# Performance work log

Hardware: AMD Instinct MI355X
Metric: run time of the kernel (lower is better)

## Reference

```python
import jax, jax.numpy as jnp
import numpy as np

NUM_BANDS = 8
WINDOW = 2048
OVERLAP = 1024
SR = 16000


def _band_mask(L):
    # Replicates torch: band = searchsorted(band_ranges, |freq|, left) - 1.
    # DC bin gives band=-1 which torch negative-indexes into the LAST band,
    # hence the mod. All bins satisfy band < NUM_BANDS, so all are assigned.
    freqs = np.fft.fftfreq(L, 1.0 / SR)
    ranges = np.linspace(0.0, SR / 2.0, NUM_BANDS + 1)
    idx = np.searchsorted(ranges, np.abs(freqs), side='left') - 1
    idx = idx % NUM_BANDS
    mask = (idx[None, :] == np.arange(NUM_BANDS)[:, None]).astype(np.float32)
    return jnp.asarray(mask)  # [bands, L]


def _band_signals(x):
    # mag*exp(i*phase) of masked bins == masked complex bins; ifft().real per band
    L = x.shape[-1]
    X = jnp.fft.fft(x)                         # [B, L] complex
    mask = _band_mask(L)                       # [bands, L]
    Xb = X[:, None, :] * mask[None, :, :]      # [B, bands, L]
    return jnp.fft.ifft(Xb).real               # [B, bands, L]


def _chunks(sig):
    L = sig.shape[-1]
    hop = WINDOW - OVERLAP
    n = (L - OVERLAP) // hop                   # num_chunks (static)
    idx = (jnp.arange(n) * hop)[:, None] + jnp.arange(WINDOW)[None, :]  # [n, W]
    return sig[:, :, idx]                       # [B, bands, n, W]


def _loudness(x):
    # BS.1770-style energy loudness (vectorized stand-in for the repo's
    # undefined `loudness` helper): -0.691 + 10*log10(mean square)
    ms = jnp.mean(x * x, axis=-1)
    return -0.691 + 10.0 * jnp.log10(ms + 1e-12)


def reference(watermarked_signals, original_signals):
    ro = _band_signals(original_signals)
    rw = _band_signals(watermarked_signals)
    lo = _loudness(_chunks(ro))                # [B, bands, n]
    lw = _loudness(_chunks(rw))
    lo = jnp.where(jnp.isnan(lo), 0.0, lo)
    lw = jnp.where(jnp.isnan(lw), 0.0, lw)
    diff = (lw - lo).reshape(-1)               # ordered (i, j, k) like the torch loop
    w = jax.nn.softmax(diff)
    return jnp.sum(w * diff)


def setup_inputs() -> dict:
    key = jax.random.key(0)
    k1, k2 = jax.random.split(key)
    B, L = 8, 160000
    return {
        'watermarked_signals': jax.random.normal(k1, (B, L), dtype=jnp.float32),
        'original_signals': jax.random.normal(k2, (B, L), dtype=jnp.float32),
    }
```

## Files before the change

kernel.cpp:

```cpp
#include <hip/hip_runtime.h>
#include <hip/hip_fp16.h>
#include <math.h>

constexpr int L      = 160000;
constexpr int BATCH  = 8;
constexpr int NB     = 8;
constexpr int NHOPS  = 156;
constexpr int NCHUNK = 155;
constexpr int RS     = 289;
constexpr float TWO_PI = 6.28318530717958647692f;
constexpr float INVL = 1.0f / (float)L;

__device__ __forceinline__ float2 cmulf(float2 a, float2 b) {
  return make_float2(a.x * b.x - a.y * b.y, a.x * b.y + a.y * b.x);
}

__device__ __forceinline__ float2 cisf(float a) {
  float s, c;
  __sincosf(a, &s, &c);
  return make_float2(c, s);
}

__device__ __forceinline__ float2 conjf(float2 a) { return make_float2(a.x, -a.y); }

__device__ __forceinline__ int pad8(int i) { return i + (i >> 3); }

template <int SIGN>
__device__ __forceinline__ void bf4s(float2* v) {
  float2 t0 = make_float2(v[0].x + v[2].x, v[0].y + v[2].y);
  float2 t1 = make_float2(v[0].x - v[2].x, v[0].y - v[2].y);
  float2 t2 = make_float2(v[1].x + v[3].x, v[1].y + v[3].y);
  float2 t3 = make_float2(v[1].x - v[3].x, v[1].y - v[3].y);
  v[0] = make_float2(t0.x + t2.x, t0.y + t2.y);
  v[2] = make_float2(t0.x - t2.x, t0.y - t2.y);
  if constexpr (SIGN < 0) {
    v[1] = make_float2(t1.x + t3.y, t1.y - t3.x);
    v[3] = make_float2(t1.x - t3.y, t1.y + t3.x);
  } else {
    v[1] = make_float2(t1.x - t3.y, t1.y + t3.x);
    v[3] = make_float2(t1.x + t3.y, t1.y - t3.x);
  }
}

template <int SIGN>
__device__ __forceinline__ void bf5s(float2* v) {
  const float c1 = 0.30901699437494745f, s1 = 0.9510565162951535f;
  const float c2 = -0.8090169943749475f, s2 = 0.5877852522924731f;
  float2 t1 = make_float2(v[1].x + v[4].x, v[1].y + v[4].y);
  float2 t3 = make_float2(v[1].x - v[4].x, v[1].y - v[4].y);
  float2 t2 = make_float2(v[2].x + v[3].x, v[2].y + v[3].y);
  float2 t4 = make_float2(v[2].x - v[3].x, v[2].y - v[3].y);
  float2 a = make_float2(v[0].x + c1 * t1.x + c2 * t2.x, v[0].y + c1 * t1.y + c2 * t2.y);
  float2 b = make_float2(s1 * t3.x + s2 * t4.x, s1 * t3.y + s2 * t4.y);
  float2 c = make_float2(v[0].x + c2 * t1.x + c1 * t2.x, v[0].y + c2 * t1.y + c1 * t2.y);
  float2 d = make_float2(s2 * t3.x - s1 * t4.x, s2 * t3.y - s1 * t4.y);
  v[0] = make_float2(v[0].x + t1.x + t2.x, v[0].y + t1.y + t2.y);
  if constexpr (SIGN < 0) {
    v[1] = make_float2(a.x + b.y, a.y - b.x);
    v[4] = make_float2(a.x - b.y, a.y + b.x);
    v[2] = make_float2(c.x + d.y, c.y - d.x);
    v[3] = make_float2(c.x - d.y, c.y + d.x);
  } else {
    v[1] = make_float2(a.x - b.y, a.y + b.x);
    v[4] = make_float2(a.x + b.y, a.y - b.x);
    v[2] = make_float2(c.x - d.y, c.y + d.x);
    v[3] = make_float2(c.x + d.y, c.y - d.x);
  }
}

template <int R>
__device__ __forceinline__ void twchain(float2* v, float2 t1) {
  float2 t = t1;
  v[1] = cmulf(v[1], t);
#pragma unroll
  for (int r = 2; r < R; ++r) { t = cmulf(t, t1); v[r] = cmulf(v[r], t); }
}

__device__ __forceinline__ int rev3_5(int q) {
  int q5 = q / 5, q25 = q / 25;
  int d0 = q - 5 * q5, d1 = q5 - 5 * q25;
  return 25 * d0 + 5 * d1 + q25;
}

__device__ __forceinline__ int rev3_4(int q) {
  return ((q & 3) << 4) | (q & 12) | (q >> 4);
}

template <int SUB, int SIGN>
__device__ __forceinline__ void dif5_stage_1b(float2* a, int idx) {
  int j = idx % SUB;
  int b = (idx / SUB) * (5 * SUB) + j;
  float2 u[5];
#pragma unroll
  for (int r = 0; r < 5; ++r) u[r] = a[b + SUB * r];
  bf5s<SIGN>(u);
  twchain<5>(u, cisf((float)SIGN * (TWO_PI / (float)(5 * SUB)) * (float)j));
#pragma unroll
  for (int r = 0; r < 5; ++r) a[b + SUB * r] = u[r];
}

template <int SUB>
__device__ __forceinline__ void dif5_ip_stage_t(float2* a, int ln, float2 t1a, float2 t1b) {
  int i1 = ln, i2 = ln + 64;
  bool g2 = (i2 < 125);
  int j1 = i1 % SUB, j2 = i2 % SUB;
  int b1 = (i1 / SUB) * (5 * SUB) + j1;
  int b2 = (i2 / SUB) * (5 * SUB) + j2;
  float2 u[5], v[5];
#pragma unroll
  for (int r = 0; r < 5; ++r) u[r] = a[b1 + SUB * r];
  if (g2) {
#pragma unroll
    for (int r = 0; r < 5; ++r) v[r] = a[b2 + SUB * r];
  }
  bf5s<1>(u);
  twchain<5>(u, t1a);
  if (g2) {
    bf5s<1>(v);
    twchain<5>(v, t1b);
  }
#pragma unroll
  for (int r = 0; r < 5; ++r) a[b1 + SUB * r] = u[r];
  if (g2) {
#pragma unroll
    for (int r = 0; r < 5; ++r) a[b2 + SUB * r] = v[r];
  }
}

template <int SIGN>
__device__ __forceinline__ void dif256sw_tw(float2* a, int ln,
                                            float2 tw1, float2 tw2, float2 tw3) {
  {
    int b = pad8(ln);
    float2 u[4];
#pragma unroll
    for (int r = 0; r < 4; ++r) u[r] = a[b + 72 * r];
    bf4s<SIGN>(u);
    twchain<4>(u, tw1);
#pragma unroll
    for (int r = 0; r < 4; ++r) a[b + 72 * r] = u[r];
  }
  {
    int j = ln & 15, b = pad8(64 * (ln >> 4) + j);
    float2 u[4];
#pragma unroll
    for (int r = 0; r < 4; ++r) u[r] = a[b + 18 * r];
    bf4s<SIGN>(u);
    twchain<4>(u, tw2);
#pragma unroll
    for (int r = 0; r < 4; ++r) a[b + 18 * r] = u[r];
  }
  {
    int j = ln & 3, jb = 16 * (ln >> 2) + j;
    float2 u[4];
#pragma unroll
    for (int r = 0; r < 4; ++r) u[r] = a[pad8(jb + 4 * r)];
    bf4s<SIGN>(u);
    twchain<4>(u, tw3);
#pragma unroll
    for (int r = 0; r < 4; ++r) a[pad8(jb + 4 * r)] = u[r];
  }
  {
    float2 u[4];
#pragma unroll
    for (int r = 0; r < 4; ++r) u[r] = a[pad8(4 * ln + r)];
    bf4s<SIGN>(u);
    int rv = rev3_4(ln);
#pragma unroll
    for (int r = 0; r < 4; ++r) a[pad8(64 * r + rv)] = u[r];
  }
}

__global__ __launch_bounds__(512) void f1_kernel(const float* __restrict__ win,
                                                 const float* __restrict__ oin,
                                                 float2* __restrict__ G,
                                                 float* __restrict__ E) {
  __shared__ float2 A[4 * 625];
  int blk = blockIdx.x;
  int tid = threadIdx.x;
  int gid = blk * 512 + tid;
  if (gid < 2 * BATCH * NB * NHOPS) E[gid] = 0.0f;
  int sig = blk >> 6, g = blk & 63;
  int n1base = g * 4;
  const float4* wp4 = (const float4*)(win + (size_t)sig * L);
  const float4* op4 = (const float4*)(oin + (size_t)sig * L);
  for (int r = tid; r < 625; r += 512) {
    float4 wv = wp4[r * 64 + g];
    float4 ov = op4[r * 64 + g];
    A[0 * 625 + r] = make_float2(wv.x, ov.x);
    A[1 * 625 + r] = make_float2(wv.y, ov.y);
    A[2 * 625 + r] = make_float2(wv.z, ov.z);
    A[3 * 625 + r] = make_float2(wv.w, ov.w);
  }
  __syncthreads();
  int col = tid >> 7, idx = tid & 127;
  float2* a = A + col * 625;
  bool act = (idx < 125);
  if (act) dif5_stage_1b<125, -1>(a, idx);
  __syncthreads();
  if (act) dif5_stage_1b<25, -1>(a, idx);
  __syncthreads();
  if (act) dif5_stage_1b<5, -1>(a, idx);
  __syncthreads();
  if (act) {
    float2 u[5];
#pragma unroll
    for (int r = 0; r < 5; ++r) u[r] = a[5 * idx + r];
    bf5s<-1>(u);
    int rv = rev3_5(idx);
#pragma unroll
    for (int r = 0; r < 5; ++r) a[125 * r + rv] = u[r];
  }
  __syncthreads();
  int cc = tid & 3, k20 = tid >> 2;
  int n1 = n1base + cc;
  float w = -(TWO_PI / (float)L) * (float)n1;
  float2 t = cisf(w * (float)k20);
  float2 stp = cisf(w * 128.0f);
  for (int k2 = k20; k2 < 625; k2 += 128) {
    G[(size_t)sig * L + k2 * 256 + n1] = cmulf(A[cc * 625 + k2], t);
    t = cmulf(t, stp);
  }
}

__global__ __launch_bounds__(1024) void fi_kernel(const float2* __restrict__ G,
                                                  __half2* __restrict__ H) {
  __shared__ float2 Xb[16 * RS];
  __shared__ float2 Wb[16 * RS];
  int blk = blockIdx.x;
  int bg  = blk / (BATCH * 40);
  int rem = blk - bg * (BATCH * 40);
  int sig = rem / 40, gr = rem % 40;
  int k2base = gr * 16;
  int tid = threadIdx.x;
  int wv = tid >> 6, ln = tid & 63;
  int k2 = k2base + wv;
  bool act = (k2 < 625);
  float2* xr = Xb + wv * RS;
  float2* wr = Wb + wv * RS;

  float2 tw1 = cisf((TWO_PI / 256.0f) * (float)ln);
  float2 tw2 = cisf((TWO_PI / 64.0f) * (float)(ln & 15));
  float2 tw3 = cisf((TWO_PI / 16.0f) * (float)(ln & 3));

  if (act) {
#pragma unroll
    for (int r = 0; r < 4; ++r)
      xr[pad8(ln + 64 * r)] = G[(size_t)sig * L + k2 * 256 + ln + 64 * r];
    dif256sw_tw<-1>(xr, ln, conjf(tw1), conjf(tw2), conjf(tw3));
  }

  int b1 = pad8(ln);
  int b2 = pad8(64 * (ln >> 4) + (ln & 15));
  int jb3 = 16 * (ln >> 2) + (ln & 3);
  int kb = 625 * ln + k2;

  int cc = tid & 15, q = tid >> 4;
  int rq = rev3_4(q);
  int k2e = k2base + cc;
  bool eact = (k2e < 625);
  float a0 = (TWO_PI / (float)L) * (float)k2e;
  float2 t0q = cisf(a0 * (float)rq);
  float2 stp = cisf(a0 * 64.0f);

#pragma unroll
  for (int bi = 0; bi < 2; ++bi) {
    int band = bg * 2 + bi;
    unsigned lo1, d1, lo2, d2;
    if (band < 7) {
      lo1 = 10000u * band + 1u;              d1 = 9999u;
      lo2 = (unsigned)L - 10000u * (band + 1); d2 = 9999u;
    } else {
      lo1 = 70001u; d1 = 19998u;
      lo2 = 0u;     d2 = 0u;
    }
    if (act) {
      float2 u[4];
#pragma unroll
      for (int r = 0; r < 4; ++r) {
        float2 x = xr[b1 + 72 * r];
        unsigned k = (unsigned)(kb + 40000 * r);
        bool in = ((k - lo1) <= d1) || ((k - lo2) <= d2);
        u[r] = in ? x : make_float2(0.0f, 0.0f);
      }
      bf4s<1>(u);
      twchain<4>(u, tw1);
#pragma unroll
      for (int r = 0; r < 4; ++r) wr[b1 + 72 * r] = u[r];
#pragma unroll
      for (int r = 0; r < 4; ++r) u[r] = wr[b2 + 18 * r];
      bf4s<1>(u);
      twchain<4>(u, tw2);
#pragma unroll
      for (int r = 0; r < 4; ++r) wr[b2 + 18 * r] = u[r];
#pragma unroll
      for (int r = 0; r < 4; ++r) u[r] = wr[pad8(jb3 + 4 * r)];
      bf4s<1>(u);
      twchain<4>(u, tw3);
#pragma unroll
      for (int r = 0; r < 4; ++r) wr[pad8(jb3 + 4 * r)] = u[r];
    }
    __syncthreads();
    if (eact) {
      size_t obase = (size_t)(sig * NB + band) * L;
      int b4 = cc * RS + pad8(4 * q);
      float2 v[4];
#pragma unroll
      for (int r = 0; r < 4; ++r) v[r] = Wb[b4 + r];
      bf4s<1>(v);
      float2 t = t0q;
#pragma unroll
      for (int r = 0; r < 4; ++r) {
        int n1 = 64 * r + rq;
        float2 val = cmulf(v[r], t);
        H[obase + (size_t)n1 * 625 + k2e] = __floats2half2_rn(val.x * INVL, val.y * INVL);
        t = cmulf(t, stp);
      }
    }
    __syncthreads();
  }
}

__global__ __launch_bounds__(256) void i2_kernel(const __half2* __restrict__ H,
                                                 float* __restrict__ E) {
  __shared__ float2 AA[4 * 625];
  __shared__ float2 AB[4 * 625];
  __shared__ float P[4 * 2 * NHOPS];
  int blk = blockIdx.x;
  int g = blk & 31, sb = blk >> 5;
  int band = sb & 7, sig = sb >> 3;
  int tid = threadIdx.x;
  int wv = tid >> 6, ln = tid & 63;
  size_t base = (size_t)(sig * NB + band) * L;
  int n1A = 8 * g + wv, n1B = 8 * g + 4 + wv;
  const __half2* HA = H + base + (size_t)n1A * 625;
  const __half2* HB = H + base + (size_t)n1B * 625;
  int j1 = ln, j2 = ln + 64;
  bool g2 = (j2 < 125);
  __half2 hA1[5], hA2[5], hB1[5], hB2[5];
#pragma unroll
  for (int r = 0; r < 5; ++r) hA1[r] = HA[j1 + 125 * r];
  if (g2) {
#pragma unroll
    for (int r = 0; r < 5; ++r) hA2[r] = HA[j2 + 125 * r];
  }
#pragma unroll
  for (int r = 0; r < 5; ++r) hB1[r] = HB[j1 + 125 * r];
  if (g2) {
#pragma unroll
    for (int r = 0; r < 5; ++r) hB2[r] = HB[j2 + 125 * r];
  }
  float2 tS1a = cisf((TWO_PI / 625.0f) * (float)j1);
  float2 tS1b = cisf((TWO_PI / 625.0f) * (float)j2);
  float2 tS2a = cisf((TWO_PI / 125.0f) * (float)(j1 % 25));
  float2 tS2b = cisf((TWO_PI / 125.0f) * (float)(j2 % 25));
  float2 tS3a = cisf((TWO_PI / 25.0f) * (float)(j1 % 5));
  float2 tS3b = cisf((TWO_PI / 25.0f) * (float)(j2 % 5));
  float2* aA = AA + wv * 625;
  float2* aB = AB + wv * 625;
  float* Pw = P + wv * (2 * NHOPS);

  {
    float2 u[5];
#pragma unroll
    for (int r = 0; r < 5; ++r) u[r] = __half22float2(hA1[r]);
    bf5s<1>(u);
    twchain<5>(u, tS1a);
#pragma unroll
    for (int r = 0; r < 5; ++r) aA[j1 + 125 * r] = u[r];
    if (g2) {
      float2 v[5];
#pragma unroll
      for (int r = 0; r < 5; ++r) v[r] = __half22float2(hA2[r]);
      bf5s<1>(v);
      twchain<5>(v, tS1b);
#pragma unroll
      for (int r = 0; r < 5; ++r) aA[j2 + 125 * r] = v[r];
    }
  }
  {
    float2 u[5];
#pragma unroll
    for (int r = 0; r < 5; ++r) u[r] = __half22float2(hB1[r]);
    bf5s<1>(u);
    twchain<5>(u, tS1a);
#pragma unroll
    for (int r = 0; r < 5; ++r) aB[j1 + 125 * r] = u[r];
    if (g2) {
      float2 v[5];
#pragma unroll
      for (int r = 0; r < 5; ++r) v[r] = __half22float2(hB2[r]);
      bf5s<1>(v);
      twchain<5>(v, tS1b);
#pragma unroll
      for (int r = 0; r < 5; ++r) aB[j2 + 125 * r] = v[r];
    }
  }
  dif5_ip_stage_t<25>(aA, ln, tS2a, tS2b);
  dif5_ip_stage_t<25>(aB, ln, tS2a, tS2b);
  dif5_ip_stage_t<5>(aA, ln, tS3a, tS3b);
  dif5_ip_stage_t<5>(aB, ln, tS3a, tS3b);
  {
    float2 u[5], v[5];
#pragma unroll
    for (int r = 0; r < 5; ++r) u[r] = aA[5 * j1 + r];
    if (g2) {
#pragma unroll
      for (int r = 0; r < 5; ++r) v[r] = aA[5 * j2 + r];
    }
    bf5s<1>(u);
    if (g2) bf5s<1>(v);
    int rv1 = rev3_5(j1), rv2 = rev3_5(j2);
#pragma unroll
    for (int r = 0; r < 5; ++r) aA[125 * r + rv1] = u[r];
    if (g2) {
#pragma unroll
      for (int r = 0; r < 5; ++r) aA[125 * r + rv2] = v[r];
    }
  }
  {
    float2 u[5], v[5];
#pragma unroll
    for (int r = 0; r < 5; ++r) u[r] = aB[5 * j1 + r];
    if (g2) {
#pragma unroll
      for (int r = 0; r < 5; ++r) v[r] = aB[5 * j2 + r];
    }
    bf5s<1>(u);
    if (g2) bf5s<1>(v);
    int rv1 = rev3_5(j1), rv2 = rev3_5(j2);
#pragma unroll
    for (int r = 0; r < 5; ++r) aB[125 * r + rv1] = u[r];
    if (g2) {
#pragma unroll
      for (int r = 0; r < 5; ++r) aB[125 * r + rv2] = v[r];
    }
  }
  for (int h = ln; h < NHOPS; h += 64) {
    float ex = 0.0f, ey = 0.0f;
#pragma unroll
    for (int d = 0; d < 4; ++d) {
      float2 zA = aA[4 * h + d];
      float2 zB = aB[4 * h + d];
      ex += zA.x * zA.x + zB.x * zB.x;
      ey += zA.y * zA.y + zB.y * zB.y;
    }
    Pw[h] = ex;
    Pw[NHOPS + h] = ey;
  }
  __syncthreads();
  int eb = (sig * NB + band) * NHOPS;
  for (int idx = tid; idx < 2 * NHOPS; idx += 256) {
    float v = P[idx] + P[2 * NHOPS + idx] + P[4 * NHOPS + idx] + P[6 * NHOPS + idx];
    int comp = idx / NHOPS, h = idx - comp * NHOPS;
    atomicAdd(&E[comp * (BATCH * NB * NHOPS) + eb + h], v);
  }
}

__global__ __launch_bounds__(1024) void finalize_kernel(const float* __restrict__ E,
                                                        float* __restrict__ out) {
  constexpr int ND = BATCH * NB * NCHUNK;
  constexpr float SC = 1.0f / 2048.0f;
  __shared__ float diffs[ND];
  __shared__ float sred[1024];
  int tid = threadIdx.x;
  for (int idx = tid; idx < ND; idx += 1024) {
    int sb = idx / NCHUNK;
    int k = idx - sb * NCHUNK;
    float msw = (E[sb * NHOPS + k] + E[sb * NHOPS + k + 1]) * SC;
    float mso = (E[64 * NHOPS + sb * NHOPS + k] + E[64 * NHOPS + sb * NHOPS + k + 1]) * SC;
    float lw = -0.691f + 10.0f * log10f(msw + 1e-12f);
    float lo = -0.691f + 10.0f * log10f(mso + 1e-12f);
    diffs[idx] = lw - lo;
  }
  __syncthreads();
  float mx = -3.4e38f;
  for (int idx = tid; idx < ND; idx += 1024) mx = fmaxf(mx, diffs[idx]);
  sred[tid] = mx;
  __syncthreads();
  for (int s = 512; s > 0; s >>= 1) {
    if (tid < s) sred[tid] = fmaxf(sred[tid], sred[tid + s]);
    __syncthreads();
  }
  float gmax = sred[0];
  __syncthreads();
  float se = 0.0f, swd = 0.0f;
  for (int idx = tid; idx < ND; idx += 1024) {
    float d = diffs[idx];
    float e = expf(d - gmax);
    se += e;
    swd += d * e;
  }
  sred[tid] = se; __syncthreads();
  for (int s = 512; s > 0; s >>= 1) { if (tid < s) sred[tid] += sred[tid + s]; __syncthreads(); }
  float tot = sred[0];
  __syncthreads();
  sred[tid] = swd; __syncthreads();
  for (int s = 512; s > 0; s >>= 1) { if (tid < s) sred[tid] += sred[tid + s]; __syncthreads(); }
  if (tid == 0) out[0] = sred[0] / tot;
}

extern "C" void kernel_launch(void* const* d_in, const int* in_sizes, int n_in,
                              void* d_out, int out_size, void* d_ws, size_t ws_size,
                              hipStream_t stream) {
  (void)in_sizes; (void)n_in; (void)out_size; (void)ws_size;
  char* ws = (char*)d_ws;
  float2*  G = (float2*)ws;
  __half2* H = (__half2*)(ws + 10240000);
  float*   E = (float*)(ws + 51200000);
  const float* w = (const float*)d_in[0];
  const float* o = (const float*)d_in[1];

  f1_kernel<<<dim3(BATCH * 64), dim3(512), 0, stream>>>(w, o, G, E);
  fi_kernel<<<dim3(4 * BATCH * 40), dim3(1024), 0, stream>>>(G, H);
  i2_kernel<<<dim3(BATCH * NB * 32), dim3(256), 0, stream>>>(H, E);
  finalize_kernel<<<dim3(1), dim3(1024), 0, stream>>>(E, (float*)d_out);
}
```

Measured before the change: 144.1 us.

## Fuse finalize into i2 via last-block counter and process four bands per fi block

```diff
diff --git a/kernel.cpp b/kernel.cpp
--- a/kernel.cpp
+++ b/kernel.cpp
@@ -174,12 +174,14 @@
 __global__ __launch_bounds__(512) void f1_kernel(const float* __restrict__ win,
                                                  const float* __restrict__ oin,
                                                  float2* __restrict__ G,
-                                                 float* __restrict__ E) {
+                                                 float* __restrict__ E,
+                                                 unsigned* __restrict__ C) {
   __shared__ float2 A[4 * 625];
   int blk = blockIdx.x;
   int tid = threadIdx.x;
   int gid = blk * 512 + tid;
   if (gid < 2 * BATCH * NB * NHOPS) E[gid] = 0.0f;
+  if (gid == 0) *C = 0u;
   int sig = blk >> 6, g = blk & 63;
   int n1base = g * 4;
   const float4* wp4 = (const float4*)(win + (size_t)sig * L);
@@ -264,8 +266,8 @@
   float2 stp = cisf(a0 * 64.0f);
 
 #pragma unroll
-  for (int bi = 0; bi < 2; ++bi) {
-    int band = bg * 2 + bi;
+  for (int bi = 0; bi < 4; ++bi) {
+    int band = bg * 4 + bi;
     unsigned lo1, d1, lo2, d2;
     if (band < 7) {
       lo1 = 10000u * band + 1u;              d1 = 9999u;
@@ -322,9 +324,10 @@
 }
 
 __global__ __launch_bounds__(256) void i2_kernel(const __half2* __restrict__ H,
-                                                 float* __restrict__ E) {
-  __shared__ float2 AA[4 * 625];
-  __shared__ float2 AB[4 * 625];
+                                                 float* __restrict__ E,
+                                                 unsigned* __restrict__ C,
+                                                 float* __restrict__ out) {
+  __shared__ float2 AB2[2][4 * 625];
   __shared__ float P[4 * 2 * NHOPS];
   int blk = blockIdx.x;
   int g = blk & 31, sb = blk >> 5;
@@ -356,8 +359,8 @@
   float2 tS2b = cisf((TWO_PI / 125.0f) * (float)(j2 % 25));
   float2 tS3a = cisf((TWO_PI / 25.0f) * (float)(j1 % 5));
   float2 tS3b = cisf((TWO_PI / 25.0f) * (float)(j2 % 5));
-  float2* aA = AA + wv * 625;
-  float2* aB = AB + wv * 625;
+  float2* aA = AB2[0] + wv * 625;
+  float2* aB = AB2[1] + wv * 625;
   float* Pw = P + wv * (2 * NHOPS);
 
   {
@@ -455,49 +458,51 @@
     int comp = idx / NHOPS, h = idx - comp * NHOPS;
     atomicAdd(&E[comp * (BATCH * NB * NHOPS) + eb + h], v);
   }
-}
-
-__global__ __launch_bounds__(1024) void finalize_kernel(const float* __restrict__ E,
-                                                        float* __restrict__ out) {
+  __threadfence();
+  __syncthreads();
+  __shared__ unsigned lastv;
+  if (tid == 0) lastv = atomicAdd(C, 1u);
+  __syncthreads();
+  if (lastv != (unsigned)(gridDim.x - 1)) return;
+  __threadfence();
+
   constexpr int ND = BATCH * NB * NCHUNK;
   constexpr float SC = 1.0f / 2048.0f;
-  __shared__ float diffs[ND];
-  __shared__ float sred[1024];
-  int tid = threadIdx.x;
-  for (int idx = tid; idx < ND; idx += 1024) {
-    int sb = idx / NCHUNK;
-    int k = idx - sb * NCHUNK;
-    float msw = (E[sb * NHOPS + k] + E[sb * NHOPS + k + 1]) * SC;
-    float mso = (E[64 * NHOPS + sb * NHOPS + k] + E[64 * NHOPS + sb * NHOPS + k + 1]) * SC;
+  float* diffs = (float*)AB2;
+  for (int idx = tid; idx < ND; idx += 256) {
+    int sb2 = idx / NCHUNK;
+    int k = idx - sb2 * NCHUNK;
+    float msw = (E[sb2 * NHOPS + k] + E[sb2 * NHOPS + k + 1]) * SC;
+    float mso = (E[64 * NHOPS + sb2 * NHOPS + k] + E[64 * NHOPS + sb2 * NHOPS + k + 1]) * SC;
     float lw = -0.691f + 10.0f * log10f(msw + 1e-12f);
     float lo = -0.691f + 10.0f * log10f(mso + 1e-12f);
     diffs[idx] = lw - lo;
   }
   __syncthreads();
   float mx = -3.4e38f;
-  for (int idx = tid; idx < ND; idx += 1024) mx = fmaxf(mx, diffs[idx]);
-  sred[tid] = mx;
-  __syncthreads();
-  for (int s = 512; s > 0; s >>= 1) {
-    if (tid < s) sred[tid] = fmaxf(sred[tid], sred[tid + s]);
+  for (int idx = tid; idx < ND; idx += 256) mx = fmaxf(mx, diffs[idx]);
+  P[tid] = mx;
+  __syncthreads();
+  for (int s = 128; s > 0; s >>= 1) {
+    if (tid < s) P[tid] = fmaxf(P[tid], P[tid + s]);
     __syncthreads();
   }
-  float gmax = sred[0];
+  float gmax = P[0];
   __syncthreads();
   float se = 0.0f, swd = 0.0f;
-  for (int idx = tid; idx < ND; idx += 1024) {
+  for (int idx = tid; idx < ND; idx += 256) {
     float d = diffs[idx];
     float e = expf(d - gmax);
     se += e;
     swd += d * e;
   }
-  sred[tid] = se; __syncthreads();
-  for (int s = 512; s > 0; s >>= 1) { if (tid < s) sred[tid] += sred[tid + s]; __syncthreads(); }
-  float tot = sred[0];
-  __syncthreads();
-  sred[tid] = swd; __syncthreads();
-  for (int s = 512; s > 0; s >>= 1) { if (tid < s) sred[tid] += sred[tid + s]; __syncthreads(); }
-  if (tid == 0) out[0] = sred[0] / tot;
+  P[tid] = se; __syncthreads();
+  for (int s = 128; s > 0; s >>= 1) { if (tid < s) P[tid] += P[tid + s]; __syncthreads(); }
+  float tot = P[0];
+  __syncthreads();
+  P[tid] = swd; __syncthreads();
+  for (int s = 128; s > 0; s >>= 1) { if (tid < s) P[tid] += P[tid + s]; __syncthreads(); }
+  if (tid == 0) out[0] = P[0] / tot;
 }
 
 extern "C" void kernel_launch(void* const* d_in, const int* in_sizes, int n_in,
@@ -505,14 +510,14 @@
                               hipStream_t stream) {
   (void)in_sizes; (void)n_in; (void)out_size; (void)ws_size;
   char* ws = (char*)d_ws;
-  float2*  G = (float2*)ws;
-  __half2* H = (__half2*)(ws + 10240000);
-  float*   E = (float*)(ws + 51200000);
+  float2*   G = (float2*)ws;
+  __half2*  H = (__half2*)(ws + 10240000);
+  float*    E = (float*)(ws + 51200000);
+  unsigned* C = (unsigned*)(ws + 51279872);
   const float* w = (const float*)d_in[0];
   const float* o = (const float*)d_in[1];
 
-  f1_kernel<<<dim3(BATCH * 64), dim3(512), 0, stream>>>(w, o, G, E);
-  fi_kernel<<<dim3(4 * BATCH * 40), dim3(1024), 0, stream>>>(G, H);
-  i2_kernel<<<dim3(BATCH * NB * 32), dim3(256), 0, stream>>>(H, E);
-  finalize_kernel<<<dim3(1), dim3(1024), 0, stream>>>(E, (float*)d_out);
-}
+  f1_kernel<<<dim3(BATCH * 64), dim3(512), 0, stream>>>(w, o, G, E, C);
+  fi_kernel<<<dim3(2 * BATCH * 40), dim3(1024), 0, stream>>>(G, H);
+  i2_kernel<<<dim3(BATCH * NB * 32), dim3(256), 0, stream>>>(H, E, C, (float*)d_out);
+}
```

Result: slower. 256.4 us (+78.0%).
